# Kernel tuning notes

Hardware: AMD Instinct MI355X
Metric: run time of the kernel (lower is better)

## Reference

```python
import jax, jax.numpy as jnp
import numpy as np

B, C, H, W = 8, 64, 32, 32
NEG = 256
TEMP = 2.0
FACTOR = 0.8
EPS = 1e-8


def setup_inputs() -> dict:
    key = jax.random.key(0)
    k1, k2, k3, k4 = jax.random.split(key, 4)
    views_1 = jax.random.normal(k1, (B, C, H, W), dtype=jnp.float32)
    views_2 = jax.random.normal(k2, (B, C, H, W), dtype=jnp.float32)
    img = jax.random.uniform(k3, (1, 3, H, W), dtype=jnp.float32)
    neg_idx = jax.random.randint(k4, (B, 2, H * W, NEG), 0, H, dtype=jnp.int32)
    return {"views_1": views_1, "views_2": views_2, "img": img, "neg_idx": neg_idx}


def _forward(views_1, views_2, img, neg_idx):
    hw = H * W
    height = jnp.arange(hw) // W
    width = jnp.arange(hw) % W
    coords = jnp.stack([height, width]).astype(jnp.float32)  # [2, hw]
    img0 = img[0]  # [3, H, W]; original uses img[0] for EVERY batch element
    euc_norm = jnp.sqrt(jnp.asarray((H - 1) ** 2 + (W - 1) ** 2, jnp.float32))
    sqrt3 = jnp.sqrt(jnp.asarray(3.0, jnp.float32))

    center = img0[:, height, width]  # [3, hw]

    def per_sample(z1, z2, nidx):
        # nidx: [2, hw, neg]
        nf = nidx.astype(jnp.float32)
        # torch.norm with no dim => scalar Frobenius norm over [2, neg] per pixel
        d = coords[:, :, None] - nf  # [2, hw, neg]
        euc = jnp.sqrt(jnp.sum(d * d, axis=(0, 2))) / euc_norm  # [hw]
        negs = img0[:, nidx[0], nidx[1]]  # [3, hw, neg]
        rd = center[:, :, None] - negs
        rgb = jnp.sqrt(jnp.sum(rd * rd, axis=(0, 2))) / sqrt3  # [hw]
        weight = euc * FACTOR + rgb * (1.0 - FACTOR)  # [hw], constant across neg

        z1v = z1.reshape(C, hw)  # [c, hw]
        pn = z2[:, nidx[0], nidx[1]]  # [c, hw, neg]
        dot = jnp.einsum('cp,cpn->pn', z1v, pn)  # [hw, neg]
        z1sq = jnp.sum(z1v * z1v, axis=0)  # [hw]
        z1n = jnp.sqrt(z1sq)
        pnn = jnp.sqrt(jnp.sum(pn * pn, axis=0))  # [hw, neg]
        cos = dot / jnp.maximum(z1n[:, None] * pnn, EPS)  # [hw, neg]
        cos0 = z1sq / jnp.maximum(z1sq, EPS)  # [hw] (self-similarity ~ 1)

        sim_neg = jnp.minimum(jnp.abs(cos * weight[:, None]), 1.0)  # [hw, neg]
        sim0 = jnp.minimum(jnp.abs(cos0), 1.0)  # [hw]
        sim = jnp.concatenate(
            [jnp.mean(sim0)[None], jnp.mean(sim_neg, axis=0) / TEMP]
        )  # [neg+1]

        # BCELoss with target = [1, 0, ..., 0]; torch clamps log terms at -100
        logp = jnp.maximum(jnp.log(sim[0]), -100.0)
        log1m = jnp.maximum(jnp.log1p(-sim[1:]), -100.0)
        bce = -(logp + jnp.sum(log1m)) / (NEG + 1)
        return bce, sim

    bce, sims = jax.vmap(per_sample)(views_1, views_2, neg_idx)
    loss = jnp.mean(bce)
    sim_all = jnp.sum(sims, axis=0)
    return (loss, sim_all[0] / B, jnp.sum(sim_all[1:]) / NEG * TEMP / B)


def reference(views_1, views_2, img, neg_idx):
    return _forward(views_1, views_2, img, neg_idx)
```

## Files before the change

### kernel.cpp

```cpp
#include <hip/hip_runtime.h>
#include <math.h>

#define BB 8
#define CC 64
#define HH 32
#define WW 32
#define HW 1024
#define NEGN 256
#define TEMP 2.0f
#define FACTOR 0.8f
#define EPSF 1e-8f
#define PT 8

__global__ __launch_bounds__(256, 4) void contrastive_fused(
    const float* __restrict__ z1,
    const float* __restrict__ z2,
    const float* __restrict__ img,
    const int*   __restrict__ nidx,
    float* __restrict__ accSim,
    float* __restrict__ accSim0)
{
    __shared__ float As_s[CC * PT];
    __shared__ float Dt_s[PT * HW];
    __shared__ float normq_s[HW];
    __shared__ float cen_s[3 * PT];
    __shared__ float z1sqs[PT];

    const int t  = threadIdx.x;
    const int b  = blockIdx.x >> 7;
    const int p0 = (blockIdx.x & 127) * PT;

    const int lane32 = t & 31;
    const int pp_b   = t >> 5;
    const int p_b    = p0 + pp_b;

    for (int i = t; i < CC * PT; i += 256) {
        const int c = i >> 3, pp = i & 7;
        As_s[i] = z1[((size_t)(b * CC + c)) * HW + p0 + pp];
    }
    if (t < 3 * PT) cen_s[t] = img[(t >> 3) * HW + p0 + (t & 7)];
    __syncthreads();

    if (t < PT) {
        float s = 0.f;
        #pragma unroll
        for (int c = 0; c < CC; ++c) { const float v = As_s[c * PT + t]; s += v * v; }
        z1sqs[t] = s;
    }

    const float4* __restrict__ z2f4 =
        reinterpret_cast<const float4*>(z2 + (size_t)b * CC * HW);

    float4 acc[PT];
    #pragma unroll
    for (int pp = 0; pp < PT; ++pp) acc[pp] = make_float4(0.f, 0.f, 0.f, 0.f);
    float4 sq = make_float4(0.f, 0.f, 0.f, 0.f);

    float4 pf[4];
    #pragma unroll
    for (int i = 0; i < 4; ++i) pf[i] = z2f4[i * (HW / 4) + t];

#define GEMM_STEP(kk, bv)                                                      \
    {                                                                          \
        sq.x = fmaf((bv).x, (bv).x, sq.x);                                     \
        sq.y = fmaf((bv).y, (bv).y, sq.y);                                     \
        sq.z = fmaf((bv).z, (bv).z, sq.z);                                     \
        sq.w = fmaf((bv).w, (bv).w, sq.w);                                     \
        const float4 a03 = reinterpret_cast<const float4*>(As_s)[(kk) * 2];    \
        const float4 a47 = reinterpret_cast<const float4*>(As_s)[(kk) * 2 + 1];\
        const float av[8] = {a03.x, a03.y, a03.z, a03.w,                       \
                             a47.x, a47.y, a47.z, a47.w};                      \
        _Pragma("unroll")                                                      \
        for (int pp = 0; pp < PT; ++pp) {                                      \
            acc[pp].x = fmaf(av[pp], (bv).x, acc[pp].x);                       \
            acc[pp].y = fmaf(av[pp], (bv).y, acc[pp].y);                       \
            acc[pp].z = fmaf(av[pp], (bv).z, acc[pp].z);                       \
            acc[pp].w = fmaf(av[pp], (bv).w, acc[pp].w);                       \
        }                                                                      \
    }

    #pragma unroll 4
    for (int k = 0; k < CC - 4; ++k) {
        const float4 bv = pf[k & 3];
        pf[k & 3] = z2f4[(k + 4) * (HW / 4) + t];
        GEMM_STEP(k, bv);
    }
    #pragma unroll
    for (int k = CC - 4; k < CC; ++k) {
        const float4 bv = pf[k & 3];
        GEMM_STEP(k, bv);
    }
#undef GEMM_STEP

    float4* Dt4 = reinterpret_cast<float4*>(Dt_s);
    #pragma unroll
    for (int pp = 0; pp < PT; ++pp) Dt4[pp * (HW / 4) + t] = acc[pp];
    reinterpret_cast<float4*>(normq_s)[t] =
        make_float4(sqrtf(sq.x), sqrtf(sq.y), sqrtf(sq.z), sqrtf(sq.w));

    int rr[8], cc_[8];
    const size_t nbase = ((size_t)(b * 2) * HW + p_b) * NEGN;
    #pragma unroll
    for (int j = 0; j < 8; ++j) {
        rr[j]  = nidx[nbase + lane32 + 32 * j];
        cc_[j] = nidx[nbase + (size_t)HW * NEGN + lane32 + 32 * j];
    }
    __syncthreads();

    const float z1sq = z1sqs[pp_b];
    const float z1n  = sqrtf(z1sq);
    const float cen0 = cen_s[pp_b], cen1 = cen_s[PT + pp_b], cen2 = cen_s[2 * PT + pp_b];
    const float hp = (float)(p_b >> 5), wp = (float)(p_b & 31);

    int   qv[8];
    float g0[8], g1[8], g2[8];
    #pragma unroll
    for (int j = 0; j < 8; ++j) {
        qv[j] = rr[j] * WW + cc_[j];
        g0[j] = img[qv[j]];
        g1[j] = img[HW + qv[j]];
        g2[j] = img[2 * HW + qv[j]];
    }
    float dotv[8], pnn[8];
    #pragma unroll
    for (int j = 0; j < 8; ++j) {
        dotv[j] = Dt_s[pp_b * HW + qv[j]];
        pnn[j]  = normq_s[qv[j]];
    }

    float se = 0.f, sr = 0.f, cosv[8];
    #pragma unroll
    for (int j = 0; j < 8; ++j) {
        const float dh = hp - (float)rr[j], dw = wp - (float)cc_[j];
        se += dh * dh + dw * dw;
        const float d0 = cen0 - g0[j];
        const float d1 = cen1 - g1[j];
        const float d2 = cen2 - g2[j];
        sr += d0 * d0 + d1 * d1 + d2 * d2;
        cosv[j] = dotv[j] / fmaxf(z1n * pnn[j], EPSF);
    }
    #pragma unroll
    for (int off = 16; off; off >>= 1) {
        se += __shfl_xor(se, off);
        sr += __shfl_xor(sr, off);
    }
    const float euc_norm = sqrtf((float)((HH - 1) * (HH - 1) + (WW - 1) * (WW - 1)));
    const float weight = sqrtf(se) / euc_norm * FACTOR +
                         sqrtf(sr) / sqrtf(3.0f) * (1.0f - FACTOR);

    float simv[8];
    #pragma unroll
    for (int j = 0; j < 8; ++j)
        simv[j] = fminf(fabsf(cosv[j] * weight), 1.0f);

    __syncthreads();
    float* simpart = Dt_s;
    #pragma unroll
    for (int j = 0; j < 8; ++j)
        simpart[pp_b * NEGN + lane32 + 32 * j] = simv[j];
    __syncthreads();

    float s = 0.f;
    #pragma unroll
    for (int pp = 0; pp < PT; ++pp) s += simpart[pp * NEGN + t];
    atomicAdd(accSim + b * NEGN + t, s);

    if (t < PT) {
        const float zz = z1sqs[t];
        const float c0 = zz / fmaxf(zz, EPSF);
        float s0 = fminf(fabsf(c0), 1.0f);
        #pragma unroll
        for (int off = 4; off; off >>= 1) s0 += __shfl_xor(s0, off);
        if (t == 0) atomicAdd(accSim0 + b, s0);
    }
}

__global__ __launch_bounds__(256) void finalize(
    const float* __restrict__ accSim,
    const float* __restrict__ accSim0,
    float* __restrict__ out)
{
    const int t = threadIdx.x;
    float ssum = 0.f, lsum = 0.f;
    #pragma unroll
    for (int b = 0; b < BB; ++b) {
        const float s = accSim[b * NEGN + t] * (1.0f / HW) * (1.0f / TEMP);
        ssum += s;
        lsum += fmaxf(log1pf(-s), -100.0f);
    }
    __shared__ float rs[4], rl[4];
    #pragma unroll
    for (int off = 32; off; off >>= 1) {
        ssum += __shfl_down(ssum, off);
        lsum += __shfl_down(lsum, off);
    }
    if ((t & 63) == 0) { rs[t >> 6] = ssum; rl[t >> 6] = lsum; }
    __syncthreads();

    if (t == 0) {
        const float S = rs[0] + rs[1] + rs[2] + rs[3];
        const float L = rl[0] + rl[1] + rl[2] + rl[3];
        float logpsum = 0.f, sim0sum = 0.f;
        #pragma unroll
        for (int b = 0; b < BB; ++b) {
            const float s0 = accSim0[b] * (1.0f / HW);
            sim0sum += s0;
            logpsum += fmaxf(logf(s0), -100.0f);
        }
        out[0] = -(logpsum + L) / ((float)(NEGN + 1) * (float)BB);
        out[1] = sim0sum / (float)BB;
        out[2] = S / (float)NEGN * TEMP / (float)BB;
    }
}

extern "C" void kernel_launch(void* const* d_in, const int* in_sizes, int n_in,
                              void* d_out, int out_size, void* d_ws, size_t ws_size,
                              hipStream_t stream) {
    const float* v1   = (const float*)d_in[0];
    const float* v2   = (const float*)d_in[1];
    const float* img  = (const float*)d_in[2];
    const int*   nidx = (const int*)  d_in[3];

    float* accSim  = (float*)d_ws;
    float* accSim0 = accSim + BB * NEGN;

    hipMemsetAsync(accSim, 0, (BB * NEGN + BB) * sizeof(float), stream);

    contrastive_fused<<<BB * (HW / PT), 256, 0, stream>>>(
        v1, v2, img, nidx, accSim, accSim0);
    finalize<<<1, 256, 0, stream>>>(accSim, accSim0, (float*)d_out);
}
```

Measured before the change: 101.9 us.

## Precompute z1 norms and packed image in prep kernel, fold cosine before gather

```diff
diff --git a/kernel.cpp b/kernel.cpp
--- a/kernel.cpp
+++ b/kernel.cpp
@@ -12,19 +12,60 @@
 #define EPSF 1e-8f
 #define PT 8
 
+
+__global__ __launch_bounds__(256) void prep(
+    const float* __restrict__ z1,
+    const float* __restrict__ img,
+    float* __restrict__ accSim,
+    float* __restrict__ accSim0,
+    float* __restrict__ z1n_ws,
+    float4* __restrict__ imgpack)
+{
+    const int b = blockIdx.x;
+    const int t = threadIdx.x;
+
+    accSim[b * NEGN + t] = 0.f;
+
+    if (t < HW / BB) {
+        const int q = b * (HW / BB) + t;
+        imgpack[q] = make_float4(img[q], img[HW + q], img[2 * HW + q], 0.f);
+    }
+
+    const float4* __restrict__ z1b =
+        reinterpret_cast<const float4*>(z1 + (size_t)b * CC * HW);
+    float4 s = make_float4(0.f, 0.f, 0.f, 0.f);
+    #pragma unroll 8
+    for (int c = 0; c < CC; ++c) {
+        const float4 v = z1b[c * (HW / 4) + t];
+        s.x = fmaf(v.x, v.x, s.x);
+        s.y = fmaf(v.y, v.y, s.y);
+        s.z = fmaf(v.z, v.z, s.z);
+        s.w = fmaf(v.w, v.w, s.w);
+    }
+    reinterpret_cast<float4*>(z1n_ws + (size_t)b * HW)[t] =
+        make_float4(sqrtf(s.x), sqrtf(s.y), sqrtf(s.z), sqrtf(s.w));
+
+    float s0 = fminf(fabsf(s.x / fmaxf(s.x, EPSF)), 1.0f)
+             + fminf(fabsf(s.y / fmaxf(s.y, EPSF)), 1.0f)
+             + fminf(fabsf(s.z / fmaxf(s.z, EPSF)), 1.0f)
+             + fminf(fabsf(s.w / fmaxf(s.w, EPSF)), 1.0f);
+    #pragma unroll
+    for (int off = 32; off; off >>= 1) s0 += __shfl_down(s0, off);
+    __shared__ float red[4];
+    if ((t & 63) == 0) red[t >> 6] = s0;
+    __syncthreads();
+    if (t == 0) accSim0[b] = red[0] + red[1] + red[2] + red[3];
+}
+
 __global__ __launch_bounds__(256, 4) void contrastive_fused(
     const float* __restrict__ z1,
     const float* __restrict__ z2,
-    const float* __restrict__ img,
     const int*   __restrict__ nidx,
-    float* __restrict__ accSim,
-    float* __restrict__ accSim0)
+    const float* __restrict__ z1n_ws,
+    const float4* __restrict__ imgpack,
+    float* __restrict__ accSim)
 {
-    __shared__ float As_s[CC * PT];
     __shared__ float Dt_s[PT * HW];
-    __shared__ float normq_s[HW];
-    __shared__ float cen_s[3 * PT];
-    __shared__ float z1sqs[PT];
 
     const int t  = threadIdx.x;
     const int b  = blockIdx.x >> 7;
@@ -34,22 +75,9 @@
     const int pp_b   = t >> 5;
     const int p_b    = p0 + pp_b;
 
-    for (int i = t; i < CC * PT; i += 256) {
-        const int c = i >> 3, pp = i & 7;
-        As_s[i] = z1[((size_t)(b * CC + c)) * HW + p0 + pp];
-    }
-    if (t < 3 * PT) cen_s[t] = img[(t >> 3) * HW + p0 + (t & 7)];
-    __syncthreads();
-
-    if (t < PT) {
-        float s = 0.f;
-        #pragma unroll
-        for (int c = 0; c < CC; ++c) { const float v = As_s[c * PT + t]; s += v * v; }
-        z1sqs[t] = s;
-    }
-
     const float4* __restrict__ z2f4 =
         reinterpret_cast<const float4*>(z2 + (size_t)b * CC * HW);
+    const float* __restrict__ z1row = z1 + (size_t)(b * CC) * HW + p0;
 
     float4 acc[PT];
     #pragma unroll
@@ -66,16 +94,13 @@
         sq.y = fmaf((bv).y, (bv).y, sq.y);                                     \
         sq.z = fmaf((bv).z, (bv).z, sq.z);                                     \
         sq.w = fmaf((bv).w, (bv).w, sq.w);                                     \
-        const float4 a03 = reinterpret_cast<const float4*>(As_s)[(kk) * 2];    \
-        const float4 a47 = reinterpret_cast<const float4*>(As_s)[(kk) * 2 + 1];\
-        const float av[8] = {a03.x, a03.y, a03.z, a03.w,                       \
-                             a47.x, a47.y, a47.z, a47.w};                      \
         _Pragma("unroll")                                                      \
         for (int pp = 0; pp < PT; ++pp) {                                      \
-            acc[pp].x = fmaf(av[pp], (bv).x, acc[pp].x);                       \
-            acc[pp].y = fmaf(av[pp], (bv).y, acc[pp].y);                       \
-            acc[pp].z = fmaf(av[pp], (bv).z, acc[pp].z);                       \
-            acc[pp].w = fmaf(av[pp], (bv).w, acc[pp].w);                       \
+            const float a = z1row[(kk) * HW + pp];      \
+            acc[pp].x = fmaf(a, (bv).x, acc[pp].x);                            \
+            acc[pp].y = fmaf(a, (bv).y, acc[pp].y);                            \
+            acc[pp].z = fmaf(a, (bv).z, acc[pp].z);                            \
+            acc[pp].w = fmaf(a, (bv).w, acc[pp].w);                            \
         }                                                                      \
     }
 
@@ -92,52 +117,70 @@
     }
 #undef GEMM_STEP
 
+    const float* __restrict__ z1nrow = z1n_ws + (size_t)b * HW + p0;
+    float z1nv[PT];
+    #pragma unroll
+    for (int pp = 0; pp < PT; ++pp) z1nv[pp] = z1nrow[pp];
+    const float4 pnn = make_float4(sqrtf(sq.x), sqrtf(sq.y),
+                                   sqrtf(sq.z), sqrtf(sq.w));
     float4* Dt4 = reinterpret_cast<float4*>(Dt_s);
     #pragma unroll
-    for (int pp = 0; pp < PT; ++pp) Dt4[pp * (HW / 4) + t] = acc[pp];
-    reinterpret_cast<float4*>(normq_s)[t] =
-        make_float4(sqrtf(sq.x), sqrtf(sq.y), sqrtf(sq.z), sqrtf(sq.w));
-
-    int rr[8], cc_[8];
+    for (int pp = 0; pp < PT; ++pp) {
+        float4 cv;
+        cv.x = acc[pp].x / fmaxf(z1nv[pp] * pnn.x, EPSF);
+        cv.y = acc[pp].y / fmaxf(z1nv[pp] * pnn.y, EPSF);
+        cv.z = acc[pp].z / fmaxf(z1nv[pp] * pnn.z, EPSF);
+        cv.w = acc[pp].w / fmaxf(z1nv[pp] * pnn.w, EPSF);
+        Dt4[pp * (HW / 4) + t] = cv;
+    }
+
     const size_t nbase = ((size_t)(b * 2) * HW + p_b) * NEGN;
-    #pragma unroll
-    for (int j = 0; j < 8; ++j) {
-        rr[j]  = nidx[nbase + lane32 + 32 * j];
-        cc_[j] = nidx[nbase + (size_t)HW * NEGN + lane32 + 32 * j];
-    }
-    __syncthreads();
-
-    const float z1sq = z1sqs[pp_b];
-    const float z1n  = sqrtf(z1sq);
-    const float cen0 = cen_s[pp_b], cen1 = cen_s[PT + pp_b], cen2 = cen_s[2 * PT + pp_b];
+    const int2* __restrict__ nr = reinterpret_cast<const int2*>(nidx + nbase);
+    const int2* __restrict__ nc =
+        reinterpret_cast<const int2*>(nidx + nbase + (size_t)HW * NEGN);
+    int2 rrv[4], ccv[4];
+    #pragma unroll
+    for (int j = 0; j < 4; ++j) {
+        rrv[j] = nr[lane32 + 32 * j];
+        ccv[j] = nc[lane32 + 32 * j];
+    }
+    __syncthreads();
+
+    const float4 cen = imgpack[p_b];
     const float hp = (float)(p_b >> 5), wp = (float)(p_b & 31);
 
-    int   qv[8];
-    float g0[8], g1[8], g2[8];
-    #pragma unroll
-    for (int j = 0; j < 8; ++j) {
-        qv[j] = rr[j] * WW + cc_[j];
-        g0[j] = img[qv[j]];
-        g1[j] = img[HW + qv[j]];
-        g2[j] = img[2 * HW + qv[j]];
-    }
-    float dotv[8], pnn[8];
-    #pragma unroll
-    for (int j = 0; j < 8; ++j) {
-        dotv[j] = Dt_s[pp_b * HW + qv[j]];
-        pnn[j]  = normq_s[qv[j]];
-    }
-
-    float se = 0.f, sr = 0.f, cosv[8];
-    #pragma unroll
-    for (int j = 0; j < 8; ++j) {
-        const float dh = hp - (float)rr[j], dw = wp - (float)cc_[j];
-        se += dh * dh + dw * dw;
-        const float d0 = cen0 - g0[j];
-        const float d1 = cen1 - g1[j];
-        const float d2 = cen2 - g2[j];
-        sr += d0 * d0 + d1 * d1 + d2 * d2;
-        cosv[j] = dotv[j] / fmaxf(z1n * pnn[j], EPSF);
+    int q[8];
+    #pragma unroll
+    for (int j = 0; j < 4; ++j) {
+        q[2 * j]     = rrv[j].x * WW + ccv[j].x;
+        q[2 * j + 1] = rrv[j].y * WW + ccv[j].y;
+    }
+    float4 g[8];
+    #pragma unroll
+    for (int e = 0; e < 8; ++e) g[e] = imgpack[q[e]];
+    float cg[8];
+    #pragma unroll
+    for (int e = 0; e < 8; ++e) cg[e] = Dt_s[pp_b * HW + q[e]];
+
+    float se = 0.f, sr = 0.f;
+    #pragma unroll
+    for (int j = 0; j < 4; ++j) {
+        {
+            const float dh = hp - (float)rrv[j].x, dw = wp - (float)ccv[j].x;
+            se += dh * dh + dw * dw;
+            const float d0 = cen.x - g[2 * j].x;
+            const float d1 = cen.y - g[2 * j].y;
+            const float d2 = cen.z - g[2 * j].z;
+            sr += d0 * d0 + d1 * d1 + d2 * d2;
+        }
+        {
+            const float dh = hp - (float)rrv[j].y, dw = wp - (float)ccv[j].y;
+            se += dh * dh + dw * dw;
+            const float d0 = cen.x - g[2 * j + 1].x;
+            const float d1 = cen.y - g[2 * j + 1].y;
+            const float d2 = cen.z - g[2 * j + 1].z;
+            sr += d0 * d0 + d1 * d1 + d2 * d2;
+        }
     }
     #pragma unroll
     for (int off = 16; off; off >>= 1) {
@@ -148,31 +191,24 @@
     const float weight = sqrtf(se) / euc_norm * FACTOR +
                          sqrtf(sr) / sqrtf(3.0f) * (1.0f - FACTOR);
 
-    float simv[8];
-    #pragma unroll
-    for (int j = 0; j < 8; ++j)
-        simv[j] = fminf(fabsf(cosv[j] * weight), 1.0f);
-
-    __syncthreads();
-    float* simpart = Dt_s;
-    #pragma unroll
-    for (int j = 0; j < 8; ++j)
-        simpart[pp_b * NEGN + lane32 + 32 * j] = simv[j];
+    float2 sv[4];
+    #pragma unroll
+    for (int j = 0; j < 4; ++j) {
+        sv[j].x = fminf(fabsf(cg[2 * j]     * weight), 1.0f);
+        sv[j].y = fminf(fabsf(cg[2 * j + 1] * weight), 1.0f);
+    }
+
+    __syncthreads();
+    float2* simpart2 = reinterpret_cast<float2*>(Dt_s);
+    #pragma unroll
+    for (int j = 0; j < 4; ++j)
+        simpart2[pp_b * (NEGN / 2) + lane32 + 32 * j] = sv[j];
     __syncthreads();
 
     float s = 0.f;
     #pragma unroll
-    for (int pp = 0; pp < PT; ++pp) s += simpart[pp * NEGN + t];
+    for (int pp = 0; pp < PT; ++pp) s += Dt_s[pp * NEGN + t];
     atomicAdd(accSim + b * NEGN + t, s);
-
-    if (t < PT) {
-        const float zz = z1sqs[t];
-        const float c0 = zz / fmaxf(zz, EPSF);
-        float s0 = fminf(fabsf(c0), 1.0f);
-        #pragma unroll
-        for (int off = 4; off; off >>= 1) s0 += __shfl_xor(s0, off);
-        if (t == 0) atomicAdd(accSim0 + b, s0);
-    }
 }
 
 __global__ __launch_bounds__(256) void finalize(
@@ -221,12 +257,14 @@
     const float* img  = (const float*)d_in[2];
     const int*   nidx = (const int*)  d_in[3];
 
-    float* accSim  = (float*)d_ws;
+    float* ws      = (float*)d_ws;
+    float* accSim  = ws;
     float* accSim0 = accSim + BB * NEGN;
-
-    hipMemsetAsync(accSim, 0, (BB * NEGN + BB) * sizeof(float), stream);
-
+    float* z1n_ws  = accSim0 + BB;
+    float4* imgpack = (float4*)(z1n_ws + BB * HW);
+
+    prep<<<BB, 256, 0, stream>>>(v1, img, accSim, accSim0, z1n_ws, imgpack);
     contrastive_fused<<<BB * (HW / PT), 256, 0, stream>>>(
-        v1, v2, img, nidx, accSim, accSim0);
+        v1, v2, nidx, z1n_ws, imgpack, accSim);
     finalize<<<1, 256, 0, stream>>>(accSim, accSim0, (float*)d_out);
 }
```

Measured after the change: 101.1 us. About the same (-0.9%).
